# Kernel optimization log

Measured on AMD Instinct MI355X. Metric: run time of the kernel, lower is better.

The kernel has to match this reference:

```python
import jax, jax.numpy as jnp
from jax import lax
import numpy as np

B, T, C = 8, 4096, 1024


def setup_inputs() -> dict:
    key = jax.random.key(0)
    ks = jax.random.split(key, 10)
    return {
        "x": jax.random.normal(ks[0], (B, T, C), jnp.float32),
        "time_decay": jax.random.uniform(ks[1], (C,), jnp.float32, -6.0, -3.0),
        "time_first": jax.random.normal(ks[2], (C,), jnp.float32) * 0.1 + 1.0,
        "time_mix_k": jax.random.uniform(ks[3], (1, 1, C), jnp.float32),
        "time_mix_v": jax.random.uniform(ks[4], (1, 1, C), jnp.float32),
        "time_mix_r": jax.random.uniform(ks[5], (1, 1, C), jnp.float32),
        "Wk": jax.random.normal(ks[6], (C, C), jnp.float32) * 0.02,
        "Wv": jax.random.normal(ks[7], (C, C), jnp.float32) * 0.02,
        "Wr": jax.random.normal(ks[8], (C, C), jnp.float32) * 0.02,
        "Wo": jax.random.normal(ks[9], (C, C), jnp.float32) * 0.02,
    }


def _wkv_scan(k, v, w, u, pp0):
    # k, v: [B, T, C]; w, u: [C]; pp0: [B, C]
    b, t, c = k.shape
    zeros = jnp.zeros((b, c), jnp.float32)

    def step(carry, kv):
        aa, bb, pp = carry
        kt, vt = kv
        ww = u + pp
        p = jnp.maximum(ww, kt)
        e1 = jnp.exp(ww - p)
        e2 = jnp.exp(kt - p)
        y = (aa * e1 + vt * e2) / (bb * e1 + e2 + 1e-6)
        ww2 = w + pp
        p2 = jnp.maximum(ww2, kt)
        e1b = jnp.exp(ww2 - p2)
        e2b = jnp.exp(kt - p2)
        return (aa * e1b + vt * e2b, bb * e1b + e2b, p2), y

    kT = jnp.swapaxes(k, 0, 1)  # [T, B, C]
    vT = jnp.swapaxes(v, 0, 1)
    _, yT = lax.scan(step, (zeros, zeros, pp0), (kT, vT))
    return jnp.swapaxes(yT, 0, 1)  # [B, T, C]


def reference(x, time_decay, time_first, time_mix_k, time_mix_v, time_mix_r, Wk, Wv, Wr, Wo):
    b, t, c = x.shape
    # time-shift: prepend zero token, drop last
    xx = jnp.concatenate([jnp.zeros((b, 1, c), x.dtype), x[:, :-1]], axis=1)
    xk = x * time_mix_k + xx * (1.0 - time_mix_k)
    xv = x * time_mix_v + xx * (1.0 - time_mix_v)
    xr = x * time_mix_r + xx * (1.0 - time_mix_r)
    k = xk @ Wk.T
    v = xv @ Wv.T
    r = jax.nn.sigmoid(xr @ Wr.T)
    w = -jnp.exp(time_decay)
    u = time_first
    pp0 = jnp.full((b, c), -1e30, jnp.float32)
    y = _wkv_scan(k, v, w, u, pp0)
    return (r * y) @ Wo.T
```

## Files before the change

kernel.cpp:

```cpp
#include <hip/hip_runtime.h>
#include <cstdint>

#define DEV __device__ __forceinline__

constexpr int Bz = 8, Tz = 4096, Cz = 1024;
constexpr int Mz = Bz * Tz;
constexpr int Sz = 32, Lz = 128;

using bf16x8  = __attribute__((ext_vector_type(8))) __bf16;
using floatx4 = __attribute__((ext_vector_type(4))) float;

DEV float bf2f(unsigned short u) { return __uint_as_float(((uint32_t)u) << 16); }
DEV unsigned short f2bf(float f) {
    uint32_t u = __float_as_uint(f);
    u += 0x7fffu + ((u >> 16) & 1u);
    return (unsigned short)(u >> 16);
}
DEV unsigned short f2h(float f) {
    _Float16 h = (_Float16)f;
    unsigned short u;
    __builtin_memcpy(&u, &h, 2);
    return u;
}
DEV float h2f(unsigned short u) {
    _Float16 h;
    __builtin_memcpy(&h, &u, 2);
    return (float)h;
}

DEV void gl2lds16(const unsigned short* g, unsigned short* l) {
    __builtin_amdgcn_global_load_lds(
        (const __attribute__((address_space(1))) void*)g,
        (__attribute__((address_space(3))) void*)l, 16, 0, 0);
}

DEV void barmem() {
    asm volatile("" ::: "memory");
    __builtin_amdgcn_s_barrier();
    asm volatile("" ::: "memory");
}

__global__ __launch_bounds__(256) void f2b_k(const float* __restrict__ w0,
                                             const float* __restrict__ w1,
                                             const float* __restrict__ w2,
                                             const float* __restrict__ w3,
                                             unsigned short* __restrict__ dst) {
    int which = blockIdx.y;
    const float* src = which == 0 ? w0 : which == 1 ? w1 : which == 2 ? w2 : w3;
    int i = blockIdx.x * 256 + threadIdx.x;
    float4 v = ((const float4*)src)[i];
    ushort4 o;
    o.x = f2bf(v.x); o.y = f2bf(v.y); o.z = f2bf(v.z); o.w = f2bf(v.w);
    ((ushort4*)(dst + (size_t)which * Cz * Cz))[i] = o;
}

DEV ushort4 mix4(float4 m, float4 xc, float4 xp) {
    ushort4 o;
    o.x = f2bf(fmaf(m.x, xc.x - xp.x, xp.x));
    o.y = f2bf(fmaf(m.y, xc.y - xp.y, xp.y));
    o.z = f2bf(fmaf(m.z, xc.z - xp.z, xp.z));
    o.w = f2bf(fmaf(m.w, xc.w - xp.w, xp.w));
    return o;
}

__global__ __launch_bounds__(256) void mix_k(const float* __restrict__ x,
    const float* __restrict__ mk, const float* __restrict__ mv, const float* __restrict__ mr,
    unsigned short* __restrict__ xk, unsigned short* __restrict__ xv,
    unsigned short* __restrict__ xr) {
    int gid = blockIdx.x * 256 + threadIdx.x;
    int m   = gid >> 8;
    int c4  = gid & 255;
    float4 xc = ((const float4*)x)[gid];
    float4 xp = make_float4(0.f, 0.f, 0.f, 0.f);
    if ((m & (Tz - 1)) != 0) xp = ((const float4*)x)[gid - 256];
    ((ushort4*)xk)[gid] = mix4(((const float4*)mk)[c4], xc, xp);
    ((ushort4*)xv)[gid] = mix4(((const float4*)mv)[c4], xc, xp);
    ((ushort4*)xr)[gid] = mix4(((const float4*)mr)[c4], xc, xp);
}

__global__ __launch_bounds__(512, 2) void gemm256(
        const unsigned short* __restrict__ A0, const unsigned short* __restrict__ A1,
        const unsigned short* __restrict__ A2,
        const unsigned short* __restrict__ Bw0, const unsigned short* __restrict__ Bw1,
        const unsigned short* __restrict__ Bw2,
        void* __restrict__ O0, void* __restrict__ O1, void* __restrict__ O2,
        int modes) {
    constexpr int Kd = 1024, Nd = 1024, NT = 16;
    __shared__ __align__(16) unsigned short lds[8 * 8192];

    const int cpx = gridDim.x >> 3;
    const int L   = (blockIdx.x & 7) * cpx + (blockIdx.x >> 3);
    const int z   = L >> 9;
    const int rr  = L & 511;
    const int m0  = (rr >> 2) << 8;
    const int n0  = (rr & 3) << 8;

    const unsigned short* A  = z == 0 ? A0  : z == 1 ? A1  : A2;
    const unsigned short* Bw = z == 0 ? Bw0 : z == 1 ? Bw1 : Bw2;
    void* Cout = z == 0 ? O0 : z == 1 ? O1 : O2;
    const int mode = (modes >> (z * 4)) & 15;

    const int tid  = threadIdx.x;
    const int lane = tid & 63;
    const int wave = tid >> 6;
    const int wr   = wave >> 2;
    const int wc   = wave & 3;
    const int l15  = lane & 15, kseg = lane >> 4;
    const int wr128 = wr * 128, wc64 = wc * 64;

    const int gi   = wave * 64 + lane;
    const int srow = gi >> 2;
    const int sg   = (gi & 3) ^ ((srow >> 1) & 3);
    const size_t sofs = (size_t)srow * Kd + sg * 8;
    const int gi8  = gi * 8;

    auto STAGE = [&](int kind, int tt) {
        const unsigned short* mat = (kind >= 2) ? Bw : A;
        const int rb = (kind >= 2) ? n0 : m0;
        const unsigned short* sb = mat + (size_t)rb * Kd + tt * 64 + (kind & 1) * 32;
        unsigned short* db = &lds[(((tt & 1) << 2) + kind) * 8192];
        gl2lds16(sb + sofs,                    db + gi8);
        gl2lds16(sb + sofs + (size_t)128 * Kd, db + gi8 + 4096);
    };

    auto LDF = [&](const unsigned short* slot, int row) -> bf16x8 {
        return *(const bf16x8*)&slot[row * 32 + ((kseg ^ ((row >> 1) & 3)) << 3)];
    };

    floatx4 acc[8][4];
#pragma unroll
    for (int mi = 0; mi < 8; mi++)
#pragma unroll
        for (int ni = 0; ni < 4; ni++) acc[mi][ni] = (floatx4){0.f, 0.f, 0.f, 0.f};

    auto QUAD = [&](const bf16x8 (&af)[4], const bf16x8 (&bfv)[4], int mo) {
#pragma unroll
        for (int i = 0; i < 4; i++)
#pragma unroll
            for (int n = 0; n < 4; n++)
                acc[mo + i][n] = __builtin_amdgcn_mfma_f32_16x16x32_bf16(
                    af[i], bfv[n], acc[mo + i][n], 0, 0, 0);
    };

    auto VMW = [&](int n) {
        if (n == 8)      { asm volatile("s_waitcnt vmcnt(8)" ::: "memory"); }
        else if (n == 4) { asm volatile("s_waitcnt vmcnt(4)" ::: "memory"); }
        else             { asm volatile("s_waitcnt vmcnt(0)" ::: "memory"); }
        __builtin_amdgcn_sched_barrier(0);
    };
    auto LKW = [&]() {
        asm volatile("s_waitcnt lgkmcnt(0)" ::: "memory");
        __builtin_amdgcn_sched_barrier(0);
    };

    auto TILE = [&](int t, bool s01, bool s23, int w1, int w2) {
        const unsigned short* Ak0 = &lds[((t & 1) << 2) * 8192];
        const unsigned short* Ak1 = Ak0 + 8192;
        const unsigned short* Bk0 = Ak0 + 2 * 8192;
        const unsigned short* Bk1 = Ak0 + 3 * 8192;
        bf16x8 fa[4], fb[4];

#pragma unroll
        for (int i = 0; i < 4; i++) {
            fa[i] = LDF(Ak0, wr128 + i * 16 + l15);
            fb[i] = LDF(Bk0, wc64 + i * 16 + l15);
        }
        if (s01) STAGE(1, t + 1);
        barmem();
        LKW();
        __builtin_amdgcn_s_setprio(1);
        QUAD(fa, fb, 0);
        __builtin_amdgcn_s_setprio(0);
        barmem();

#pragma unroll
        for (int i = 0; i < 4; i++)
            fa[i] = LDF(Ak0, wr128 + 64 + i * 16 + l15);
        if (s01) STAGE(3, t + 1);
        barmem();
        LKW();
        __builtin_amdgcn_s_setprio(1);
        QUAD(fa, fb, 4);
        __builtin_amdgcn_s_setprio(0);
        VMW(w1);
        barmem();

#pragma unroll
        for (int i = 0; i < 4; i++) {
            fa[i] = LDF(Ak1, wr128 + i * 16 + l15);
            fb[i] = LDF(Bk1, wc64 + i * 16 + l15);
        }
        if (s23) STAGE(0, t + 2);
        barmem();
        LKW();
        __builtin_amdgcn_s_setprio(1);
        QUAD(fa, fb, 0);
        __builtin_amdgcn_s_setprio(0);
        barmem();

#pragma unroll
        for (int i = 0; i < 4; i++)
            fa[i] = LDF(Ak1, wr128 + 64 + i * 16 + l15);
        if (s23) STAGE(2, t + 2);
        barmem();
        LKW();
        __builtin_amdgcn_s_setprio(1);
        QUAD(fa, fb, 4);
        __builtin_amdgcn_s_setprio(0);
        if (w2 >= 0) VMW(w2);
        barmem();
    };

    STAGE(0, 0); STAGE(2, 0);
    STAGE(1, 0); STAGE(3, 0);
    STAGE(0, 1); STAGE(2, 1);
    VMW(8);
    barmem();

#pragma unroll 2
    for (int t = 0; t < NT - 2; t++)
        TILE(t, true, true, 8, 8);
    TILE(NT - 2, true, false, 8, 4);
    TILE(NT - 1, false, false, 0, -1);

    const int cr = kseg * 4;
#pragma unroll
    for (int mi = 0; mi < 8; mi++) {
#pragma unroll
        for (int ni = 0; ni < 4; ni++) {
            size_t row = (size_t)(m0 + wr128 + mi * 16 + cr);
            size_t col = (size_t)(n0 + wc64 + ni * 16 + l15);
#pragma unroll
            for (int rg = 0; rg < 4; rg++) {
                float v = acc[mi][ni][rg];
                size_t idx = (row + rg) * Nd + col;
                if (mode == 0) {
                    ((float*)Cout)[idx] = v;
                } else if (mode == 1) {
                    ((unsigned short*)Cout)[idx] = f2bf(v);
                } else if (mode == 2) {
                    float sg2 = 1.0f / (1.0f + __expf(-v));
                    ((unsigned short*)Cout)[idx] = f2bf(sg2);
                } else {
                    ((unsigned short*)Cout)[idx] = f2h(v);
                }
            }
        }
    }
}

__global__ __launch_bounds__(256) void wkv_pass1(const unsigned short* __restrict__ kh,
    const unsigned short* __restrict__ vb, const float* __restrict__ td,
    float2* __restrict__ SA, float2* __restrict__ SB) {
    int tid = blockIdx.x * 256 + threadIdx.x;
    int c2  = tid & 511;
    int bs  = tid >> 9;
    int b   = bs >> 5, s = bs & (Sz - 1);
    int c   = c2 * 2;
    float lam0 = __expf(-__expf(td[c]));
    float lam1 = __expf(-__expf(td[c + 1]));
    size_t base = (((size_t)(b * Tz + s * Lz)) * Cz + c) >> 1;
    float pa0 = 0.f, pb0 = 0.f, pa1 = 0.f, pb1 = 0.f;
#pragma unroll 4
    for (int i = 0; i < Lz; i++) {
        size_t idx = base + (size_t)i * (Cz / 2);
        ushort2 kk = ((const ushort2*)kh)[idx];
        ushort2 vv = ((const ushort2*)vb)[idx];
        float e0 = __expf(h2f(kk.x)), e1 = __expf(h2f(kk.y));
        pa0 = fmaf(pa0, lam0, e0 * bf2f(vv.x));
        pb0 = fmaf(pb0, lam0, e0);
        pa1 = fmaf(pa1, lam1, e1 * bf2f(vv.y));
        pb1 = fmaf(pb1, lam1, e1);
    }
    SA[tid] = make_float2(pa0, pa1);
    SB[tid] = make_float2(pb0, pb1);
}

__global__ __launch_bounds__(256) void wkv_pass2(const float* __restrict__ td,
                                                 float2* __restrict__ SA,
                                                 float2* __restrict__ SB) {
    int tid = blockIdx.x * 256 + threadIdx.x;
    int c2  = tid & 511;
    int b   = tid >> 9;
    int c   = c2 * 2;
    float lamL0 = __expf(-__expf(td[c]) * (float)Lz);
    float lamL1 = __expf(-__expf(td[c + 1]) * (float)Lz);
    float A0 = 0.f, B0 = 0.f, A1 = 0.f, B1 = 0.f;
    for (int s = 0; s < Sz; s++) {
        size_t idx = ((size_t)(b * Sz + s)) * 512 + c2;
        float2 ta = SA[idx], tb = SB[idx];
        SA[idx] = make_float2(A0, A1);
        SB[idx] = make_float2(B0, B1);
        A0 = fmaf(A0, lamL0, ta.x);  B0 = fmaf(B0, lamL0, tb.x);
        A1 = fmaf(A1, lamL1, ta.y);  B1 = fmaf(B1, lamL1, tb.y);
    }
}

__global__ __launch_bounds__(256) void wkv_pass3(const unsigned short* __restrict__ kh,
    const unsigned short* __restrict__ vb, const unsigned short* __restrict__ rb,
    const float* __restrict__ td, const float* __restrict__ tf,
    const float2* __restrict__ SA, const float2* __restrict__ SB,
    unsigned short* __restrict__ ry) {
    int tid = blockIdx.x * 256 + threadIdx.x;
    int c2  = tid & 511;
    int bs  = tid >> 9;
    int b   = bs >> 5, s = bs & (Sz - 1);
    int c   = c2 * 2;
    float lam0 = __expf(-__expf(td[c]));
    float lam1 = __expf(-__expf(td[c + 1]));
    float eu0  = __expf(tf[c]);
    float eu1  = __expf(tf[c + 1]);
    float2 fa = SA[tid], fb = SB[tid];
    float A0 = fa.x, A1 = fa.y, B0 = fb.x, B1 = fb.y;
    size_t base = (((size_t)(b * Tz + s * Lz)) * Cz + c) >> 1;
#pragma unroll 2
    for (int i = 0; i < Lz; i++) {
        size_t idx = base + (size_t)i * (Cz / 2);
        ushort2 kk = ((const ushort2*)kh)[idx];
        ushort2 vv = ((const ushort2*)vb)[idx];
        ushort2 rr = ((const ushort2*)rb)[idx];
        float e0 = __expf(h2f(kk.x)), e1 = __expf(h2f(kk.y));
        float ev0 = e0 * bf2f(vv.x), ev1 = e1 * bf2f(vv.y);
        float y0 = fmaf(A0, eu0, ev0) * __builtin_amdgcn_rcpf(fmaf(B0, eu0, e0));
        float y1 = fmaf(A1, eu1, ev1) * __builtin_amdgcn_rcpf(fmaf(B1, eu1, e1));
        ushort2 o;
        o.x = f2bf(bf2f(rr.x) * y0);
        o.y = f2bf(bf2f(rr.y) * y1);
        ((ushort2*)ry)[idx] = o;
        A0 = fmaf(A0, lam0, ev0);  B0 = fmaf(B0, lam0, e0);
        A1 = fmaf(A1, lam1, ev1);  B1 = fmaf(B1, lam1, e1);
    }
}

extern "C" void kernel_launch(void* const* d_in, const int* in_sizes, int n_in,
                              void* d_out, int out_size, void* d_ws, size_t ws_size,
                              hipStream_t stream) {
    const float* x  = (const float*)d_in[0];
    const float* td = (const float*)d_in[1];
    const float* tf = (const float*)d_in[2];
    const float* mk = (const float*)d_in[3];
    const float* mv = (const float*)d_in[4];
    const float* mr = (const float*)d_in[5];
    const float* Wk = (const float*)d_in[6];
    const float* Wv = (const float*)d_in[7];
    const float* Wr = (const float*)d_in[8];
    const float* Wo = (const float*)d_in[9];

    constexpr size_t SZ_BF = (size_t)Mz * Cz * 2;
    constexpr size_t SZ_W  = (size_t)Cz * Cz * 2;
    constexpr size_t SZ_S  = (size_t)Bz * Sz * Cz * 4;

    char* ws = (char*)d_ws;
    unsigned short* xk  = (unsigned short*)(ws);
    unsigned short* xv  = (unsigned short*)(ws + SZ_BF);
    unsigned short* xr  = (unsigned short*)(ws + 2 * SZ_BF);
    unsigned short* kf  = (unsigned short*)(ws + 3 * SZ_BF);
    unsigned short* vb  = (unsigned short*)(ws + 4 * SZ_BF);
    unsigned short* rb  = (unsigned short*)(ws + 5 * SZ_BF);
    unsigned short* wts = (unsigned short*)(ws + 6 * SZ_BF);
    float2*         SA  = (float2*)        (ws + 6 * SZ_BF + 4 * SZ_W);
    float2*         SB  = (float2*)        (ws + 6 * SZ_BF + 4 * SZ_W + SZ_S);
    unsigned short* wkb = wts;
    unsigned short* wvb = wts + (size_t)Cz * Cz;
    unsigned short* wrb = wts + (size_t)2 * Cz * Cz;
    unsigned short* wob = wts + (size_t)3 * Cz * Cz;
    unsigned short* ry  = xk;

    f2b_k<<<dim3(Cz * Cz / 4 / 256, 4), dim3(256), 0, stream>>>(Wk, Wv, Wr, Wo, wts);

    mix_k<<<dim3(Mz * Cz / 4 / 256), dim3(256), 0, stream>>>(x, mk, mv, mr, xk, xv, xr);

    gemm256<<<dim3(512 * 3), dim3(512), 0, stream>>>(
        xk, xv, xr, wkb, wvb, wrb, (void*)kf, (void*)vb, (void*)rb,
        (3) | (1 << 4) | (2 << 8));

    wkv_pass1<<<dim3(Bz * Sz * Cz / 2 / 256), dim3(256), 0, stream>>>(kf, vb, td, SA, SB);
    wkv_pass2<<<dim3(Bz * Cz / 2 / 256), dim3(256), 0, stream>>>(td, SA, SB);
    wkv_pass3<<<dim3(Bz * Sz * Cz / 2 / 256), dim3(256), 0, stream>>>(kf, vb, rb, td, tf,
                                                                      SA, SB, ry);

    gemm256<<<dim3(512), dim3(512), 0, stream>>>(
        ry, ry, ry, wob, wob, wob, d_out, d_out, d_out, 0);
}
```

Before: 703.2 us.

## Merge half-tile MFMA phases and drop intermediate barriers in GEMM main loop

Each k-subtile now preloads both A fragment halves into separate registers, issues both global-to-LDS stages together, and runs the two MFMA quads back to back. This removes two workgroup barriers and LDS waits per subtile. It also removes the sched_barrier pins after the waitcnt helpers so the compiler can interleave loads and MFMAs. The cost is extra VGPRs for the second A fragment set, and a risk of LDS hazards now that fewer barriers order the staging writes against fragment reads.

```diff
diff --git a/kernel.cpp b/kernel.cpp
--- a/kernel.cpp
+++ b/kernel.cpp
@@ -146,11 +146,9 @@
         if (n == 8)      { asm volatile("s_waitcnt vmcnt(8)" ::: "memory"); }
         else if (n == 4) { asm volatile("s_waitcnt vmcnt(4)" ::: "memory"); }
         else             { asm volatile("s_waitcnt vmcnt(0)" ::: "memory"); }
-        __builtin_amdgcn_sched_barrier(0);
     };
     auto LKW = [&]() {
         asm volatile("s_waitcnt lgkmcnt(0)" ::: "memory");
-        __builtin_amdgcn_sched_barrier(0);
     };
 
     auto TILE = [&](int t, bool s01, bool s23, int w1, int w2) {
@@ -158,30 +156,22 @@
         const unsigned short* Ak1 = Ak0 + 8192;
         const unsigned short* Bk0 = Ak0 + 2 * 8192;
         const unsigned short* Bk1 = Ak0 + 3 * 8192;
-        bf16x8 fa[4], fb[4];
+        bf16x8 fa[4], fb[4], ga[4];
 
 #pragma unroll
         for (int i = 0; i < 4; i++) {
             fa[i] = LDF(Ak0, wr128 + i * 16 + l15);
             fb[i] = LDF(Bk0, wc64 + i * 16 + l15);
         }
-        if (s01) STAGE(1, t + 1);
-        barmem();
-        LKW();
+#pragma unroll
+        for (int i = 0; i < 4; i++)
+            ga[i] = LDF(Ak0, wr128 + 64 + i * 16 + l15);
+        if (s01) { STAGE(1, t + 1); STAGE(3, t + 1); }
         __builtin_amdgcn_s_setprio(1);
         QUAD(fa, fb, 0);
+        QUAD(ga, fb, 4);
         __builtin_amdgcn_s_setprio(0);
-        barmem();
-
-#pragma unroll
-        for (int i = 0; i < 4; i++)
-            fa[i] = LDF(Ak0, wr128 + 64 + i * 16 + l15);
-        if (s01) STAGE(3, t + 1);
-        barmem();
         LKW();
-        __builtin_amdgcn_s_setprio(1);
-        QUAD(fa, fb, 4);
-        __builtin_amdgcn_s_setprio(0);
         VMW(w1);
         barmem();
 
@@ -190,25 +180,16 @@
             fa[i] = LDF(Ak1, wr128 + i * 16 + l15);
             fb[i] = LDF(Bk1, wc64 + i * 16 + l15);
         }
-        if (s23) STAGE(0, t + 2);
-        barmem();
-        LKW();
+#pragma unroll
+        for (int i = 0; i < 4; i++)
+            ga[i] = LDF(Ak1, wr128 + 64 + i * 16 + l15);
+        if (s23) { STAGE(0, t + 2); STAGE(2, t + 2); }
         __builtin_amdgcn_s_setprio(1);
         QUAD(fa, fb, 0);
+        QUAD(ga, fb, 4);
         __builtin_amdgcn_s_setprio(0);
-        barmem();
-
-#pragma unroll
-        for (int i = 0; i < 4; i++)
-            fa[i] = LDF(Ak1, wr128 + 64 + i * 16 + l15);
-        if (s23) STAGE(2, t + 2);
-        barmem();
         LKW();
-        __builtin_amdgcn_s_setprio(1);
-        QUAD(fa, fb, 4);
-        __builtin_amdgcn_s_setprio(0);
-        if (w2 >= 0) VMW(w2);
-        barmem();
+        if (w2 >= 0) { VMW(w2); barmem(); }
     };
 
     STAGE(0, 0); STAGE(2, 0);
```

New measurement: 736.4 us. 4.7% more time.

## Double-buffer MFMA fragments to overlap LDS reads with matrix math

Applied to the files above, without the earlier changes.

Restructures the GEMM tile loop so LDS fragment loads for the next quarter-step are issued before the current QUAD of MFMAs runs, using two register sets (aX/aY, bX/bY). It drops the explicit lgkmcnt(0) waits that stalled before each MFMA block and retunes the vmcnt waits to match the new staging order. The goal is to hide LDS latency behind matrix-core work. The cost is higher VGPR pressure and reliance on the compiler to insert correct LDS waits, with possible races around the barriers.

```diff
diff --git a/kernel.cpp b/kernel.cpp
--- a/kernel.cpp
+++ b/kernel.cpp
@@ -144,84 +144,85 @@
 
     auto VMW = [&](int n) {
         if (n == 8)      { asm volatile("s_waitcnt vmcnt(8)" ::: "memory"); }
+        else if (n == 6) { asm volatile("s_waitcnt vmcnt(6)" ::: "memory"); }
         else if (n == 4) { asm volatile("s_waitcnt vmcnt(4)" ::: "memory"); }
         else             { asm volatile("s_waitcnt vmcnt(0)" ::: "memory"); }
-        __builtin_amdgcn_sched_barrier(0);
-    };
-    auto LKW = [&]() {
-        asm volatile("s_waitcnt lgkmcnt(0)" ::: "memory");
-        __builtin_amdgcn_sched_barrier(0);
-    };
-
-    auto TILE = [&](int t, bool s01, bool s23, int w1, int w2) {
-        const unsigned short* Ak0 = &lds[((t & 1) << 2) * 8192];
-        const unsigned short* Ak1 = Ak0 + 8192;
-        const unsigned short* Bk0 = Ak0 + 2 * 8192;
-        const unsigned short* Bk1 = Ak0 + 3 * 8192;
-        bf16x8 fa[4], fb[4];
-
-#pragma unroll
-        for (int i = 0; i < 4; i++) {
-            fa[i] = LDF(Ak0, wr128 + i * 16 + l15);
-            fb[i] = LDF(Bk0, wc64 + i * 16 + l15);
-        }
-        if (s01) STAGE(1, t + 1);
-        barmem();
-        LKW();
-        __builtin_amdgcn_s_setprio(1);
-        QUAD(fa, fb, 0);
-        __builtin_amdgcn_s_setprio(0);
-        barmem();
-
-#pragma unroll
-        for (int i = 0; i < 4; i++)
-            fa[i] = LDF(Ak0, wr128 + 64 + i * 16 + l15);
-        if (s01) STAGE(3, t + 1);
-        barmem();
-        LKW();
-        __builtin_amdgcn_s_setprio(1);
-        QUAD(fa, fb, 4);
-        __builtin_amdgcn_s_setprio(0);
-        VMW(w1);
-        barmem();
-
-#pragma unroll
-        for (int i = 0; i < 4; i++) {
-            fa[i] = LDF(Ak1, wr128 + i * 16 + l15);
-            fb[i] = LDF(Bk1, wc64 + i * 16 + l15);
-        }
-        if (s23) STAGE(0, t + 2);
-        barmem();
-        LKW();
-        __builtin_amdgcn_s_setprio(1);
-        QUAD(fa, fb, 0);
-        __builtin_amdgcn_s_setprio(0);
-        barmem();
-
-#pragma unroll
-        for (int i = 0; i < 4; i++)
-            fa[i] = LDF(Ak1, wr128 + 64 + i * 16 + l15);
-        if (s23) STAGE(2, t + 2);
-        barmem();
-        LKW();
-        __builtin_amdgcn_s_setprio(1);
-        QUAD(fa, fb, 4);
-        __builtin_amdgcn_s_setprio(0);
-        if (w2 >= 0) VMW(w2);
-        barmem();
-    };
+    };
+
+    bf16x8 aX[4], aY[4], bX[4], bY[4];
 
     STAGE(0, 0); STAGE(2, 0);
     STAGE(1, 0); STAGE(3, 0);
     STAGE(0, 1); STAGE(2, 1);
     VMW(8);
     barmem();
+    {
+        const unsigned short* Ak0_ = &lds[0];
+        const unsigned short* Bk0_ = &lds[2 * 8192];
+#pragma unroll
+        for (int i = 0; i < 4; i++) {
+            aX[i] = LDF(Ak0_, wr128 + i * 16 + l15);
+            bX[i] = LDF(Bk0_, wc64 + i * 16 + l15);
+        }
+    }
+
+    auto TILE = [&](int t, bool s01, bool s23, int w0, int w2, bool last) {
+        const unsigned short* Ak0 = &lds[((t & 1) << 2) * 8192];
+        const unsigned short* Ak1 = Ak0 + 8192;
+        const unsigned short* Bk1 = Ak0 + 3 * 8192;
+        const unsigned short* Ak0n = &lds[(((t + 1) & 1) << 2) * 8192];
+        const unsigned short* Bk0n = Ak0n + 2 * 8192;
+
+#pragma unroll
+        for (int i = 0; i < 4; i++)
+            aY[i] = LDF(Ak0, wr128 + 64 + i * 16 + l15);
+        if (s01) STAGE(1, t + 1);
+        __builtin_amdgcn_s_setprio(1);
+        QUAD(aX, bX, 0);
+        __builtin_amdgcn_s_setprio(0);
+        VMW(w0);
+        barmem();
+
+#pragma unroll
+        for (int i = 0; i < 4; i++) {
+            aX[i] = LDF(Ak1, wr128 + i * 16 + l15);
+            bY[i] = LDF(Bk1, wc64 + i * 16 + l15);
+        }
+        if (s01) STAGE(3, t + 1);
+        __builtin_amdgcn_s_setprio(1);
+        QUAD(aY, bX, 4);
+        __builtin_amdgcn_s_setprio(0);
+        barmem();
+
+#pragma unroll
+        for (int i = 0; i < 4; i++)
+            aY[i] = LDF(Ak1, wr128 + 64 + i * 16 + l15);
+        if (s23) STAGE(0, t + 2);
+        __builtin_amdgcn_s_setprio(1);
+        QUAD(aX, bY, 0);
+        __builtin_amdgcn_s_setprio(0);
+        if (w2 >= 0) VMW(w2);
+        barmem();
+
+        if (!last) {
+#pragma unroll
+            for (int i = 0; i < 4; i++) {
+                aX[i] = LDF(Ak0n, wr128 + i * 16 + l15);
+                bX[i] = LDF(Bk0n, wc64 + i * 16 + l15);
+            }
+        }
+        if (s23) STAGE(2, t + 2);
+        __builtin_amdgcn_s_setprio(1);
+        QUAD(aY, bY, 4);
+        __builtin_amdgcn_s_setprio(0);
+        if (!last) barmem();
+    };
 
 #pragma unroll 2
     for (int t = 0; t < NT - 2; t++)
-        TILE(t, true, true, 8, 8);
-    TILE(NT - 2, true, false, 8, 4);
-    TILE(NT - 1, false, false, 0, -1);
+        TILE(t, true, true, 6, 6, false);
+    TILE(NT - 2, true, false, 6, 4, false);
+    TILE(NT - 1, false, false, 0, -1, true);
 
     const int cr = kseg * 4;
 #pragma unroll
```

After: 705.3 us. About the same (+0.3%).
